# Performance work log

Hardware: AMD Instinct MI355X
Metric: run time of the kernel (lower is better)

Reference implementation:

```python
import jax, jax.numpy as jnp
import numpy as np

N = 100000
D_IN = 256
C = 4          # num_classes
D_C = 32       # output_dim // num_classes
E = 1600000    # nnz per class adjacency


def setup_inputs() -> dict:
    key = jax.random.key(0)
    k1, k2, k3, k4, k5 = jax.random.split(key, 5)
    x = jax.random.normal(k1, (N, D_IN), dtype=jnp.float32)
    # kernel (input_dim, output_dim) split along axis=1 into C chunks -> [D_IN, C, D_C]
    W = jax.random.normal(k2, (D_IN, C, D_C), dtype=jnp.float32) * (2.0 / D_IN) ** 0.5
    rows = jax.random.randint(k3, (C, E), 0, N, dtype=jnp.int64)
    cols = jax.random.randint(k4, (C, E), 0, N, dtype=jnp.int64)
    vals = jax.random.uniform(k5, (C, E), dtype=jnp.float32)
    return {"x": x, "W": W, "rows": rows, "cols": cols, "vals": vals}


def reference(x, W, rows, cols, vals):
    # dropout with rate 0.0 is identity.
    n = x.shape[0]
    # per-class dense transform: tmp[:, c, :] = x @ W[:, c, :]
    tmp = jnp.einsum('nd,dcf->ncf', x, W)  # [N, C, D_C]

    def prop(r, c, v, t):
        # t: [N, D_C] features for one class; SpMM A_c @ t via gather+segment_sum
        msg = t[c] * v[:, None]                              # [E, D_C]
        return jax.ops.segment_sum(msg, r, num_segments=n)   # [N, D_C]

    out = jax.vmap(prop, in_axes=(0, 0, 0, 1))(rows, cols, vals, tmp)  # [C, N, D_C]
    z = jnp.transpose(out, (1, 0, 2)).reshape(n, -1)  # concat along feature axis -> [N, C*D_C]
    return jax.nn.relu(z)
```

## Files before the change

kernel.cpp:

```cpp
#include <hip/hip_runtime.h>
#include <hip/hip_bf16.h>
#include <hip/hip_fp16.h>

#define D_IN 256
#define D_OUT 128
#define D_C 32
#define NUM_C 4
#define RB_LOG 10
#define RB 1024
#define MB_MAX 400

typedef _Float16 f16x8 __attribute__((ext_vector_type(8)));
typedef float    f32x4 __attribute__((ext_vector_type(4)));

__global__ void wcvt_kernel(const float* __restrict__ W, __half* __restrict__ Wt) {
    int t = blockIdx.x * 256 + threadIdx.x;
    if (t >= D_IN * D_OUT) return;
    int col = t >> 8;
    int k   = t & 255;
    Wt[col * D_IN + k] = __float2half(W[k * D_OUT + col]);
}

__global__ __launch_bounds__(256) void bucket_hist_kernel(const int* __restrict__ rows,
                                                          int* __restrict__ bcnt,
                                                          int CE, int E, int NB, int MB) {
    __shared__ int h[MB_MAX];
    const int t = threadIdx.x;
    for (int i = t; i < MB; i += 256) h[i] = 0;
    __syncthreads();
    const int CE4 = CE >> 2;
    const int4* rows4 = reinterpret_cast<const int4*>(rows);
    int base4 = blockIdx.x * 4096;
    #pragma unroll 4
    for (int i = 0; i < 16; ++i) {
        int i4 = base4 + t + i * 256;
        if (i4 < CE4) {
            int e0 = i4 << 2;
            int c = (e0 >= 3 * E) ? 3 : (e0 >= 2 * E) ? 2 : (e0 >= E) ? 1 : 0;
            int4 rv = rows4[i4];
            atomicAdd(&h[c * NB + (rv.x >> RB_LOG)], 1);
            atomicAdd(&h[c * NB + (rv.y >> RB_LOG)], 1);
            atomicAdd(&h[c * NB + (rv.z >> RB_LOG)], 1);
            atomicAdd(&h[c * NB + (rv.w >> RB_LOG)], 1);
        }
    }
    if (blockIdx.x == 0 && t < (CE & 3)) {
        int e = (CE4 << 2) + t;
        int c = (e >= 3 * E) ? 3 : (e >= 2 * E) ? 2 : (e >= E) ? 1 : 0;
        atomicAdd(&h[c * NB + (rows[e] >> RB_LOG)], 1);
    }
    __syncthreads();
    for (int i = t; i < MB; i += 256)
        if (h[i]) atomicAdd(&bcnt[i], h[i]);
}

__global__ __launch_bounds__(512) void bucket_scan_kernel(const int* __restrict__ bcnt,
                                                          int* __restrict__ bstartP,
                                                          int* __restrict__ bheadLine,
                                                          int* __restrict__ bstartD,
                                                          int* __restrict__ starts,
                                                          int MB, int M, int slackLines) {
    __shared__ int sd[512];
    int t = threadIdx.x;
    int v = (t < MB) ? bcnt[t] : 0;
    int capL = ((v + 7) >> 3) + slackLines;
    sd[t] = capL; __syncthreads();
    for (int off = 1; off < 512; off <<= 1) {
        int add = (t >= off) ? sd[t - off] : 0;
        __syncthreads();
        sd[t] += add;
        __syncthreads();
    }
    int exclL = sd[t] - capL;
    if (t < MB) { bstartP[t] = exclL * 8; bheadLine[t] = exclL; }
    __syncthreads();
    sd[t] = v; __syncthreads();
    for (int off = 1; off < 512; off <<= 1) {
        int add = (t >= off) ? sd[t - off] : 0;
        __syncthreads();
        sd[t] += add;
        __syncthreads();
    }
    int exclD = sd[t] - v;
    if (t < MB) bstartD[t] = exclD;
    if (t == 511) starts[M] = sd[511];
}

__global__ __launch_bounds__(512) void part_gemm_kernel(const int* __restrict__ rows,
                                                        const int* __restrict__ cols,
                                                        const float* __restrict__ vals,
                                                        int* __restrict__ bheadLine,
                                                        int2* __restrict__ arena,
                                                        int CE, int E, int NB, int MB,
                                                        int partBlocks,
                                                        const float* __restrict__ x,
                                                        const __half* __restrict__ Wt,
                                                        __half* __restrict__ tmp,
                                                        int Nrows) {
    __shared__ __align__(16) char smem[65536];
    const int t = threadIdx.x;

    if (blockIdx.x < partBlocks) {
        int* lcnt  = (int*)smem;
        int* lbase = lcnt + MB_MAX;
        for (int i = t; i < MB; i += 512) lcnt[i] = 0;
        __syncthreads();
        const int base = blockIdx.x * 8192;
        const int end  = min(base + 8192, CE);

        {
            int nvec4 = (end - base) >> 2;
            const int4* rows4 = reinterpret_cast<const int4*>(rows + base);
            #pragma unroll 4
            for (int i = 0; i < 4; ++i) {
                int i4 = t + i * 512;
                if (i4 < nvec4) {
                    int e0 = base + (i4 << 2);
                    int c = (e0 >= 3 * E) ? 3 : (e0 >= 2 * E) ? 2 : (e0 >= E) ? 1 : 0;
                    int4 rv = rows4[i4];
                    atomicAdd(&lcnt[c * NB + (rv.x >> RB_LOG)], 1);
                    atomicAdd(&lcnt[c * NB + (rv.y >> RB_LOG)], 1);
                    atomicAdd(&lcnt[c * NB + (rv.z >> RB_LOG)], 1);
                    atomicAdd(&lcnt[c * NB + (rv.w >> RB_LOG)], 1);
                }
            }
            int e = base + (nvec4 << 2) + t;
            if (e < end) {
                int c = (e >= 3 * E) ? 3 : (e >= 2 * E) ? 2 : (e >= E) ? 1 : 0;
                atomicAdd(&lcnt[c * NB + (rows[e] >> RB_LOG)], 1);
            }
        }
        __syncthreads();

        for (int b = t; b < MB; b += 512) {
            int n = lcnt[b];
            lbase[b] = n ? atomicAdd(&bheadLine[b], (n + 7) >> 3) * 8 : 0;
        }
        __syncthreads();
        for (int i = t; i < MB; i += 512) lcnt[i] = 0;
        __syncthreads();

        for (int i = 0; i < 16; ++i) {
            int e = base + t + i * 512;
            if (e < end) {
                int c = (e >= 3 * E) ? 3 : (e >= 2 * E) ? 2 : (e >= E) ? 1 : 0;
                int r = rows[e];
                int b = c * NB + (r >> RB_LOG);
                int rank = atomicAdd(&lcnt[b], 1);
                arena[lbase[b] + rank] = make_int2(cols[e] | ((r & (RB - 1)) << 17),
                                                   __float_as_int(vals[e]));
            }
        }
        __syncthreads();

        for (int b = t; b < MB; b += 512) {
            int n = lcnt[b];
            if (n) {
                int endp = ((n + 7) >> 3) * 8;
                for (int s2 = n; s2 < endp; ++s2)
                    arena[lbase[b] + s2] = make_int2(-1, 0);
            }
        }
    } else {
        f16x8* As = (f16x8*)smem;
        const int brow = (blockIdx.x - partBlocks) * 128;
        const int w   = t >> 6;
        const int cls = w & 3;
        const int rh  = w >> 2;
        const int l   = t & 63;
        const int l15 = l & 15;
        const int hi  = l >> 4;

        f16x8 bf[8][2];
        #pragma unroll
        for (int ks = 0; ks < 8; ++ks)
            #pragma unroll
            for (int cti = 0; cti < 2; ++cti)
                bf[ks][cti] = *reinterpret_cast<const f16x8*>(
                    Wt + (size_t)((cls * 2 + cti) * 16 + l15) * D_IN + ks * 32 + hi * 8);

        #pragma unroll
        for (int i = 0; i < 8; ++i) {
            int ci  = i * 512 + t;
            int row = ci >> 5;
            int kc  = ci & 31;
            int grow = brow + row;
            float4 a0 = make_float4(0.f, 0.f, 0.f, 0.f);
            float4 a1 = make_float4(0.f, 0.f, 0.f, 0.f);
            if (grow < Nrows) {
                const float* src = x + (size_t)grow * D_IN + kc * 8;
                a0 = *reinterpret_cast<const float4*>(src);
                a1 = *reinterpret_cast<const float4*>(src + 4);
            }
            f16x8 hh;
            hh[0] = (_Float16)a0.x; hh[1] = (_Float16)a0.y;
            hh[2] = (_Float16)a0.z; hh[3] = (_Float16)a0.w;
            hh[4] = (_Float16)a1.x; hh[5] = (_Float16)a1.y;
            hh[6] = (_Float16)a1.z; hh[7] = (_Float16)a1.w;
            As[kc * 128 + (row ^ kc)] = hh;
        }
        __syncthreads();

        f32x4 acc[4][2] = {};
        #pragma unroll
        for (int rt = 0; rt < 4; ++rt) {
            const int arow = rh * 64 + rt * 16 + l15;
            #pragma unroll
            for (int ks = 0; ks < 8; ++ks) {
                const int kcA = ks * 4 + hi;
                f16x8 afrag = As[kcA * 128 + (arow ^ kcA)];
                acc[rt][0] = __builtin_amdgcn_mfma_f32_16x16x32_f16(afrag, bf[ks][0], acc[rt][0], 0, 0, 0);
                acc[rt][1] = __builtin_amdgcn_mfma_f32_16x16x32_f16(afrag, bf[ks][1], acc[rt][1], 0, 0, 0);
            }
        }

        #pragma unroll
        for (int rt = 0; rt < 4; ++rt)
            #pragma unroll
            for (int cti = 0; cti < 2; ++cti) {
                const int cio = cti * 16 + l15;
                #pragma unroll
                for (int r = 0; r < 4; ++r) {
                    int grow = brow + rh * 64 + rt * 16 + hi * 4 + r;
                    if (grow < Nrows)
                        tmp[((size_t)cls * Nrows + grow) * 32 + cio] = __float2half((float)acc[rt][cti][r]);
                }
            }
    }
}

__global__ __launch_bounds__(1024) void rowsort_kernel(const int* __restrict__ bstartP,
                                                       const int* __restrict__ bheadLine,
                                                       const int* __restrict__ bstartD,
                                                       const int2* __restrict__ src,
                                                       unsigned* __restrict__ dst,
                                                       int* __restrict__ starts,
                                                       int N, int NB) {
    __shared__ int lcnt[RB];
    __shared__ int sd[RB];
    int b = blockIdx.x;
    int c = b / NB, rb = b - c * NB;
    int t = threadIdx.x;
    int s = bstartP[b];
    int nspan = bheadLine[b] * 8 - s;
    int dbase = bstartD[b];

    lcnt[t] = 0;
    __syncthreads();
    for (int i = t; i < nspan; i += 1024) {
        unsigned u = (unsigned)src[s + i].x;
        if ((u & 0x1FFFFu) != 0x1FFFFu)
            atomicAdd(&lcnt[(u >> 17) & (RB - 1)], 1);
    }
    __syncthreads();
    int v = lcnt[t];
    sd[t] = v; __syncthreads();
    for (int off = 1; off < 1024; off <<= 1) {
        int add = (t >= off) ? sd[t - off] : 0;
        __syncthreads();
        sd[t] += add;
        __syncthreads();
    }
    int excl = sd[t] - v;
    int grow = (rb << RB_LOG) + t;
    if (grow < N) starts[c * N + grow] = dbase + excl;
    __syncthreads();
    lcnt[t] = excl;
    __syncthreads();
    for (int i = t; i < nspan; i += 1024) {
        int2 rec = src[s + i];
        unsigned u = (unsigned)rec.x;
        if ((u & 0x1FFFFu) != 0x1FFFFu) {
            int rl  = (u >> 17) & (RB - 1);
            int pos = atomicAdd(&lcnt[rl], 1);
            __half h = __float2half(__int_as_float(rec.y));
            unsigned hb = (unsigned)*reinterpret_cast<unsigned short*>(&h);
            dst[dbase + pos] = (hb << 17) | (u & 0x1FFFFu);
        }
    }
}

__global__ __launch_bounds__(256) void pull2_kernel(const int* __restrict__ starts,
                                                    const unsigned* __restrict__ arena,
                                                    const uint2* __restrict__ tmp4,
                                                    float* __restrict__ out,
                                                    int N, int M) {
    int p = blockIdx.x * 32 + (threadIdx.x >> 3);
    if (p >= M) return;
    const int lf = threadIdx.x & 7;
    int c   = p / N;
    int row = p - c * N;
    int s = starts[p];
    int n = starts[p + 1] - s;
    const uint2* tc = tmp4 + (size_t)c * N * 8 + lf;

    float4 acc = make_float4(0.f, 0.f, 0.f, 0.f);
    int base = 0;
    for (; base + 16 <= n; base += 16) {
        unsigned r[16];
        #pragma unroll
        for (int j = 0; j < 16; ++j) r[j] = arena[s + base + j];
        #pragma unroll
        for (int j = 0; j < 16; ++j) {
            unsigned short hb = (unsigned short)(r[j] >> 17);
            float v = __half2float(*reinterpret_cast<__half*>(&hb));
            uint2 tw = tc[(size_t)(r[j] & 0x1FFFFu) * 8];
            float2 t0 = __half22float2(*reinterpret_cast<__half2*>(&tw.x));
            float2 t1 = __half22float2(*reinterpret_cast<__half2*>(&tw.y));
            acc.x = fmaf(v, t0.x, acc.x);
            acc.y = fmaf(v, t0.y, acc.y);
            acc.z = fmaf(v, t1.x, acc.z);
            acc.w = fmaf(v, t1.y, acc.w);
        }
    }
    if (base + 8 <= n) {
        unsigned r[8];
        #pragma unroll
        for (int j = 0; j < 8; ++j) r[j] = arena[s + base + j];
        #pragma unroll
        for (int j = 0; j < 8; ++j) {
            unsigned short hb = (unsigned short)(r[j] >> 17);
            float v = __half2float(*reinterpret_cast<__half*>(&hb));
            uint2 tw = tc[(size_t)(r[j] & 0x1FFFFu) * 8];
            float2 t0 = __half22float2(*reinterpret_cast<__half2*>(&tw.x));
            float2 t1 = __half22float2(*reinterpret_cast<__half2*>(&tw.y));
            acc.x = fmaf(v, t0.x, acc.x);
            acc.y = fmaf(v, t0.y, acc.y);
            acc.z = fmaf(v, t1.x, acc.z);
            acc.w = fmaf(v, t1.y, acc.w);
        }
        base += 8;
    }
    for (; base < n; ++base) {
        unsigned u = arena[s + base];
        unsigned short hb = (unsigned short)(u >> 17);
        float v = __half2float(*reinterpret_cast<__half*>(&hb));
        uint2 tw = tc[(size_t)(u & 0x1FFFFu) * 8];
        float2 t0 = __half22float2(*reinterpret_cast<__half2*>(&tw.x));
        float2 t1 = __half22float2(*reinterpret_cast<__half2*>(&tw.y));
        acc.x = fmaf(v, t0.x, acc.x);
        acc.y = fmaf(v, t0.y, acc.y);
        acc.z = fmaf(v, t1.x, acc.z);
        acc.w = fmaf(v, t1.y, acc.w);
    }
    *reinterpret_cast<float4*>(&out[(size_t)row * D_OUT + c * D_C + 4 * lf]) =
        make_float4(fmaxf(acc.x, 0.f), fmaxf(acc.y, 0.f),
                    fmaxf(acc.z, 0.f), fmaxf(acc.w, 0.f));
}

__global__ __launch_bounds__(256) void scatter_kernel(const int* __restrict__ rows,
                                                      const int* __restrict__ cols,
                                                      const float* __restrict__ vals,
                                                      const __half* __restrict__ tmp,
                                                      float* __restrict__ out,
                                                      long long totalEdges, int E, int N) {
    long long gid = (long long)blockIdx.x * 8 + (threadIdx.x >> 5);
    if (gid >= totalEdges) return;
    const int lane = threadIdx.x & 31;
    const long long e1 = E, e2 = 2LL * E, e3 = 3LL * E;
    int c = (gid >= e3) ? 3 : (gid >= e2) ? 2 : (gid >= e1) ? 1 : 0;
    const float tv = __half2float(tmp[((size_t)c * N + cols[gid]) * 32 + lane]);
    atomicAdd(&out[(size_t)rows[gid] * D_OUT + c * D_C + lane], tv * vals[gid]);
}

__global__ void relu_kernel(float* __restrict__ out, int n4) {
    int i = blockIdx.x * blockDim.x + threadIdx.x;
    if (i < n4) {
        float4 v = reinterpret_cast<float4*>(out)[i];
        v.x = fmaxf(v.x, 0.f); v.y = fmaxf(v.y, 0.f);
        v.z = fmaxf(v.z, 0.f); v.w = fmaxf(v.w, 0.f);
        reinterpret_cast<float4*>(out)[i] = v;
    }
}

extern "C" void kernel_launch(void* const* d_in, const int* in_sizes, int n_in,
                              void* d_out, int out_size, void* d_ws, size_t ws_size,
                              hipStream_t stream) {
    const float* x    = (const float*)d_in[0];
    const float* W    = (const float*)d_in[1];
    const int*   rows = (const int*)d_in[2];
    const int*   cols = (const int*)d_in[3];
    const float* vals = (const float*)d_in[4];
    float* out = (float*)d_out;

    const int N  = in_sizes[0] / D_IN;
    const int CE = in_sizes[2];
    const int E  = CE / NUM_C;
    const int NB = (N + RB - 1) >> RB_LOG;
    const int MB = NUM_C * NB;
    const int M  = NUM_C * N;

    const int partBlocks = (CE + 8191) / 8192;
    const int gemmBlocks = (N + 127) / 128;
    const int slackLines = (7 * partBlocks + 7) / 8 + 1;
    const long long capRecs = (long long)((CE + 7) & ~7) + (long long)MB * slackLines * 8 + (long long)MB * 8;

    size_t off = 0;
    __half* tmp  = (__half*)((char*)d_ws + off); off += (size_t)N * D_OUT * 2;
    off = (off + 15) & ~(size_t)15;
    __half* Wt   = (__half*)((char*)d_ws + off); off += (size_t)D_IN * D_OUT * 2;
    int* bcnt    = (int*)((char*)d_ws + off);   off += (size_t)MB * 4;
    int* bstartP = (int*)((char*)d_ws + off);   off += (size_t)MB * 4;
    int* bheadL  = (int*)((char*)d_ws + off);   off += (size_t)MB * 4;
    int* bstartD = (int*)((char*)d_ws + off);   off += (size_t)MB * 4;
    int* starts  = (int*)((char*)d_ws + off);   off += (size_t)(M + 1) * 4;
    off = (off + 63) & ~(size_t)63;
    int2* arena  = (int2*)((char*)d_ws + off);  off += (size_t)capRecs * 8;
    unsigned* sorted = (unsigned*)((char*)d_ws + off); off += (size_t)CE * 4;
    const bool ok = (off <= ws_size) && (MB <= MB_MAX) && (MB <= 512);

    wcvt_kernel<<<(D_IN * D_OUT + 255) / 256, 256, 0, stream>>>(W, Wt);

    if (ok) {
        hipMemsetAsync(bcnt, 0, (size_t)MB * 4, stream);
        const int histBlocks = ((CE >> 2) + 4095) / 4096;
        bucket_hist_kernel<<<histBlocks, 256, 0, stream>>>(rows, bcnt, CE, E, NB, MB);
        bucket_scan_kernel<<<1, 512, 0, stream>>>(bcnt, bstartP, bheadL, bstartD, starts, MB, M, slackLines);
        part_gemm_kernel<<<partBlocks + gemmBlocks, 512, 0, stream>>>(
            rows, cols, vals, bheadL, arena, CE, E, NB, MB, partBlocks, x, Wt, tmp, N);
        rowsort_kernel<<<MB, 1024, 0, stream>>>(bstartP, bheadL, bstartD, arena, sorted, starts, N, NB);
        const int pullBlocks = (M + 31) / 32;
        pull2_kernel<<<pullBlocks, 256, 0, stream>>>(starts, sorted,
                                                     reinterpret_cast<const uint2*>(tmp), out, N, M);
    } else {
        part_gemm_kernel<<<gemmBlocks, 512, 0, stream>>>(
            rows, cols, vals, bheadL, arena, CE, E, NB, MB, 0, x, Wt, tmp, N);
        hipMemsetAsync(d_out, 0, (size_t)out_size * sizeof(float), stream);
        const int scatterBlocks = (CE + 7) / 8;
        scatter_kernel<<<scatterBlocks, 256, 0, stream>>>(rows, cols, vals, tmp, out, (long long)CE, E, N);
        const int n4 = out_size / 4;
        relu_kernel<<<(n4 + 255) / 256, 256, 0, stream>>>(out, n4);
    }
}
```

Baseline: 274.8 us.

## Interleave partition and GEMM blocks and halve GEMM row tile

The fused partition/GEMM launch now interleaves block roles: every third block does edge partitioning and the other two do GEMM work. Before, all partition blocks came first and all GEMM blocks after. The GEMM tile shrinks from 128 to 64 rows, and shared memory drops from 64KB to 32KB, so more blocks can be resident per CU. The aim is to overlap the atomic- and memory-bound partitioning with the MFMA-bound transform, instead of running them as two phases. Correctness relies on the grid being sized so that twice the partition block count covers all GEMM tiles, which holds for these shapes but is not checked in general.

```diff
diff --git a/kernel.cpp b/kernel.cpp
--- a/kernel.cpp
+++ b/kernel.cpp
@@ -92,20 +92,34 @@
                                                         int* __restrict__ bheadLine,
                                                         int2* __restrict__ arena,
                                                         int CE, int E, int NB, int MB,
-                                                        int partBlocks,
+                                                        int partBlocks, int gemmBlocks,
                                                         const float* __restrict__ x,
                                                         const __half* __restrict__ Wt,
                                                         __half* __restrict__ tmp,
                                                         int Nrows) {
-    __shared__ __align__(16) char smem[65536];
+    __shared__ __align__(16) char smem[32768];
     const int t = threadIdx.x;
-
-    if (blockIdx.x < partBlocks) {
+    const int bid = blockIdx.x;
+
+    bool isPart; int pidx, gidx;
+    if (partBlocks > 0) {
+        isPart = (bid % 3) == 0;
+        pidx = bid / 3;
+        gidx = bid - pidx - 1;
+        if (isPart && pidx >= partBlocks) return;
+        if (!isPart && gidx >= gemmBlocks) return;
+    } else {
+        isPart = false;
+        gidx = bid;
+        if (gidx >= gemmBlocks) return;
+    }
+
+    if (isPart) {
         int* lcnt  = (int*)smem;
         int* lbase = lcnt + MB_MAX;
         for (int i = t; i < MB; i += 512) lcnt[i] = 0;
         __syncthreads();
-        const int base = blockIdx.x * 8192;
+        const int base = pidx * 8192;
         const int end  = min(base + 8192, CE);
 
         {
@@ -124,7 +138,7 @@
                     atomicAdd(&lcnt[c * NB + (rv.w >> RB_LOG)], 1);
                 }
             }
-            int e = base + (nvec4 << 2) + t;
+            int e = base + (((end - base) >> 2) << 2) + t;
             if (e < end) {
                 int c = (e >= 3 * E) ? 3 : (e >= 2 * E) ? 2 : (e >= E) ? 1 : 0;
                 atomicAdd(&lcnt[c * NB + (rows[e] >> RB_LOG)], 1);
@@ -163,7 +177,7 @@
         }
     } else {
         f16x8* As = (f16x8*)smem;
-        const int brow = (blockIdx.x - partBlocks) * 128;
+        const int brow = gidx * 64;
         const int w   = t >> 6;
         const int cls = w & 3;
         const int rh  = w >> 2;
@@ -180,7 +194,7 @@
                     Wt + (size_t)((cls * 2 + cti) * 16 + l15) * D_IN + ks * 32 + hi * 8);
 
         #pragma unroll
-        for (int i = 0; i < 8; ++i) {
+        for (int i = 0; i < 4; ++i) {
             int ci  = i * 512 + t;
             int row = ci >> 5;
             int kc  = ci & 31;
@@ -197,31 +211,31 @@
             hh[2] = (_Float16)a0.z; hh[3] = (_Float16)a0.w;
             hh[4] = (_Float16)a1.x; hh[5] = (_Float16)a1.y;
             hh[6] = (_Float16)a1.z; hh[7] = (_Float16)a1.w;
-            As[kc * 128 + (row ^ kc)] = hh;
-        }
-        __syncthreads();
-
-        f32x4 acc[4][2] = {};
-        #pragma unroll
-        for (int rt = 0; rt < 4; ++rt) {
-            const int arow = rh * 64 + rt * 16 + l15;
+            As[kc * 64 + (row ^ kc)] = hh;
+        }
+        __syncthreads();
+
+        f32x4 acc[2][2] = {};
+        #pragma unroll
+        for (int rt = 0; rt < 2; ++rt) {
+            const int arow = rh * 32 + rt * 16 + l15;
             #pragma unroll
             for (int ks = 0; ks < 8; ++ks) {
                 const int kcA = ks * 4 + hi;
-                f16x8 afrag = As[kcA * 128 + (arow ^ kcA)];
+                f16x8 afrag = As[kcA * 64 + (arow ^ kcA)];
                 acc[rt][0] = __builtin_amdgcn_mfma_f32_16x16x32_f16(afrag, bf[ks][0], acc[rt][0], 0, 0, 0);
                 acc[rt][1] = __builtin_amdgcn_mfma_f32_16x16x32_f16(afrag, bf[ks][1], acc[rt][1], 0, 0, 0);
             }
         }
 
         #pragma unroll
-        for (int rt = 0; rt < 4; ++rt)
+        for (int rt = 0; rt < 2; ++rt)
             #pragma unroll
             for (int cti = 0; cti < 2; ++cti) {
                 const int cio = cti * 16 + l15;
                 #pragma unroll
                 for (int r = 0; r < 4; ++r) {
-                    int grow = brow + rh * 64 + rt * 16 + hi * 4 + r;
+                    int grow = brow + rh * 32 + rt * 16 + hi * 4 + r;
                     if (grow < Nrows)
                         tmp[((size_t)cls * Nrows + grow) * 32 + cio] = __float2half((float)acc[rt][cti][r]);
                 }
@@ -391,7 +405,7 @@
     const int M  = NUM_C * N;
 
     const int partBlocks = (CE + 8191) / 8192;
-    const int gemmBlocks = (N + 127) / 128;
+    const int gemmBlocks = (N + 63) / 64;
     const int slackLines = (7 * partBlocks + 7) / 8 + 1;
     const long long capRecs = (long long)((CE + 7) & ~7) + (long long)MB * slackLines * 8 + (long long)MB * 8;
 
@@ -416,15 +430,16 @@
         const int histBlocks = ((CE >> 2) + 4095) / 4096;
         bucket_hist_kernel<<<histBlocks, 256, 0, stream>>>(rows, bcnt, CE, E, NB, MB);
         bucket_scan_kernel<<<1, 512, 0, stream>>>(bcnt, bstartP, bheadL, bstartD, starts, MB, M, slackLines);
-        part_gemm_kernel<<<partBlocks + gemmBlocks, 512, 0, stream>>>(
-            rows, cols, vals, bheadL, arena, CE, E, NB, MB, partBlocks, x, Wt, tmp, N);
+        const int totalBlocks = 3 * partBlocks;
+        part_gemm_kernel<<<totalBlocks, 512, 0, stream>>>(
+            rows, cols, vals, bheadL, arena, CE, E, NB, MB, partBlocks, gemmBlocks, x, Wt, tmp, N);
         rowsort_kernel<<<MB, 1024, 0, stream>>>(bstartP, bheadL, bstartD, arena, sorted, starts, N, NB);
         const int pullBlocks = (M + 31) / 32;
         pull2_kernel<<<pullBlocks, 256, 0, stream>>>(starts, sorted,
                                                      reinterpret_cast<const uint2*>(tmp), out, N, M);
     } else {
         part_gemm_kernel<<<gemmBlocks, 512, 0, stream>>>(
-            rows, cols, vals, bheadL, arena, CE, E, NB, MB, 0, x, Wt, tmp, N);
+            rows, cols, vals, bheadL, arena, CE, E, NB, MB, 0, gemmBlocks, x, Wt, tmp, N);
         hipMemsetAsync(d_out, 0, (size_t)out_size * sizeof(float), stream);
         const int scatterBlocks = (CE + 7) / 8;
         scatter_kernel<<<scatterBlocks, 256, 0, stream>>>(rows, cols, vals, tmp, out, (long long)CE, E, N);
```

Result: slower. 287.3 us (+4.5%).

## Split partition arena into packed records and row-local array, stash rows in registers

Applied to the files above, without the earlier changes.

The partition stage now writes a 4-byte packed record (fp16 value and column) plus a separate 2-byte local-row array, replacing the 8-byte int2 arena, and moves fp16 conversion earlier. Allocation granularity changes from 8-record lines to 16-record units. The row-sort kernel reads only the 2-byte row array for its histogram, keeps those row ids in a register stash for the scatter pass, and copies the precomputed records directly. The aim is to cut arena write and read traffic. The cost is extra register pressure from the stash and somewhat more padding slack.

```diff
diff --git a/kernel.cpp b/kernel.cpp
--- a/kernel.cpp
+++ b/kernel.cpp
@@ -9,6 +9,7 @@
 #define RB_LOG 10
 #define RB 1024
 #define MB_MAX 400
+#define RSTASH 24
 
 typedef _Float16 f16x8 __attribute__((ext_vector_type(8)));
 typedef float    f32x4 __attribute__((ext_vector_type(4)));
@@ -55,24 +56,24 @@
 }
 
 __global__ __launch_bounds__(512) void bucket_scan_kernel(const int* __restrict__ bcnt,
-                                                          int* __restrict__ bstartP,
-                                                          int* __restrict__ bheadLine,
+                                                          int* __restrict__ bstartU,
+                                                          int* __restrict__ bheadU,
                                                           int* __restrict__ bstartD,
                                                           int* __restrict__ starts,
-                                                          int MB, int M, int slackLines) {
+                                                          int MB, int M, int slackUnits) {
     __shared__ int sd[512];
     int t = threadIdx.x;
     int v = (t < MB) ? bcnt[t] : 0;
-    int capL = ((v + 7) >> 3) + slackLines;
-    sd[t] = capL; __syncthreads();
+    int capU = ((v + 15) >> 4) + slackUnits;
+    sd[t] = capU; __syncthreads();
     for (int off = 1; off < 512; off <<= 1) {
         int add = (t >= off) ? sd[t - off] : 0;
         __syncthreads();
         sd[t] += add;
         __syncthreads();
     }
-    int exclL = sd[t] - capL;
-    if (t < MB) { bstartP[t] = exclL * 8; bheadLine[t] = exclL; }
+    int exclU = sd[t] - capU;
+    if (t < MB) { bstartU[t] = exclU; bheadU[t] = exclU; }
     __syncthreads();
     sd[t] = v; __syncthreads();
     for (int off = 1; off < 512; off <<= 1) {
@@ -89,8 +90,9 @@
 __global__ __launch_bounds__(512) void part_gemm_kernel(const int* __restrict__ rows,
                                                         const int* __restrict__ cols,
                                                         const float* __restrict__ vals,
-                                                        int* __restrict__ bheadLine,
-                                                        int2* __restrict__ arena,
+                                                        int* __restrict__ bheadU,
+                                                        unsigned* __restrict__ rec,
+                                                        unsigned short* __restrict__ rl,
                                                         int CE, int E, int NB, int MB,
                                                         int partBlocks,
                                                         const float* __restrict__ x,
@@ -124,7 +126,7 @@
                     atomicAdd(&lcnt[c * NB + (rv.w >> RB_LOG)], 1);
                 }
             }
-            int e = base + (nvec4 << 2) + t;
+            int e = base + (((end - base) >> 2) << 2) + t;
             if (e < end) {
                 int c = (e >= 3 * E) ? 3 : (e >= 2 * E) ? 2 : (e >= E) ? 1 : 0;
                 atomicAdd(&lcnt[c * NB + (rows[e] >> RB_LOG)], 1);
@@ -134,7 +136,7 @@
 
         for (int b = t; b < MB; b += 512) {
             int n = lcnt[b];
-            lbase[b] = n ? atomicAdd(&bheadLine[b], (n + 7) >> 3) * 8 : 0;
+            lbase[b] = n ? atomicAdd(&bheadU[b], (n + 15) >> 4) * 16 : 0;
         }
         __syncthreads();
         for (int i = t; i < MB; i += 512) lcnt[i] = 0;
@@ -147,8 +149,11 @@
                 int r = rows[e];
                 int b = c * NB + (r >> RB_LOG);
                 int rank = atomicAdd(&lcnt[b], 1);
-                arena[lbase[b] + rank] = make_int2(cols[e] | ((r & (RB - 1)) << 17),
-                                                   __float_as_int(vals[e]));
+                int pos = lbase[b] + rank;
+                __half h = __float2half(vals[e]);
+                unsigned hb = (unsigned)*reinterpret_cast<unsigned short*>(&h);
+                rec[pos] = (hb << 17) | (unsigned)cols[e];
+                rl[pos]  = (unsigned short)(r & (RB - 1));
             }
         }
         __syncthreads();
@@ -156,9 +161,9 @@
         for (int b = t; b < MB; b += 512) {
             int n = lcnt[b];
             if (n) {
-                int endp = ((n + 7) >> 3) * 8;
+                int endp = ((n + 15) >> 4) << 4;
                 for (int s2 = n; s2 < endp; ++s2)
-                    arena[lbase[b] + s2] = make_int2(-1, 0);
+                    rl[lbase[b] + s2] = 0xFFFFu;
             }
         }
     } else {
@@ -229,10 +234,11 @@
     }
 }
 
-__global__ __launch_bounds__(1024) void rowsort_kernel(const int* __restrict__ bstartP,
-                                                       const int* __restrict__ bheadLine,
+__global__ __launch_bounds__(1024) void rowsort_kernel(const int* __restrict__ bstartU,
+                                                       const int* __restrict__ bheadU,
                                                        const int* __restrict__ bstartD,
-                                                       const int2* __restrict__ src,
+                                                       const unsigned short* __restrict__ rl,
+                                                       const unsigned* __restrict__ rec,
                                                        unsigned* __restrict__ dst,
                                                        int* __restrict__ starts,
                                                        int N, int NB) {
@@ -241,16 +247,25 @@
     int b = blockIdx.x;
     int c = b / NB, rb = b - c * NB;
     int t = threadIdx.x;
-    int s = bstartP[b];
-    int nspan = bheadLine[b] * 8 - s;
+    int s = bstartU[b] * 16;
+    int span = bheadU[b] * 16 - s;
     int dbase = bstartD[b];
 
+    unsigned short st[RSTASH];
     lcnt[t] = 0;
     __syncthreads();
-    for (int i = t; i < nspan; i += 1024) {
-        unsigned u = (unsigned)src[s + i].x;
-        if ((u & 0x1FFFFu) != 0x1FFFFu)
-            atomicAdd(&lcnt[(u >> 17) & (RB - 1)], 1);
+    #pragma unroll
+    for (int k = 0; k < RSTASH; ++k) {
+        int i = t + k * 1024;
+        if (i < span) {
+            unsigned short r = rl[s + i];
+            st[k] = r;
+            if (r < RB) atomicAdd(&lcnt[r], 1);
+        }
+    }
+    for (int i = t + RSTASH * 1024; i < span; i += 1024) {
+        unsigned short r = rl[s + i];
+        if (r < RB) atomicAdd(&lcnt[r], 1);
     }
     __syncthreads();
     int v = lcnt[t];
@@ -267,15 +282,22 @@
     __syncthreads();
     lcnt[t] = excl;
     __syncthreads();
-    for (int i = t; i < nspan; i += 1024) {
-        int2 rec = src[s + i];
-        unsigned u = (unsigned)rec.x;
-        if ((u & 0x1FFFFu) != 0x1FFFFu) {
-            int rl  = (u >> 17) & (RB - 1);
-            int pos = atomicAdd(&lcnt[rl], 1);
-            __half h = __float2half(__int_as_float(rec.y));
-            unsigned hb = (unsigned)*reinterpret_cast<unsigned short*>(&h);
-            dst[dbase + pos] = (hb << 17) | (u & 0x1FFFFu);
+    #pragma unroll
+    for (int k = 0; k < RSTASH; ++k) {
+        int i = t + k * 1024;
+        if (i < span) {
+            unsigned short r = st[k];
+            if (r < RB) {
+                int pos = atomicAdd(&lcnt[r], 1);
+                dst[dbase + pos] = rec[s + i];
+            }
+        }
+    }
+    for (int i = t + RSTASH * 1024; i < span; i += 1024) {
+        unsigned short r = rl[s + i];
+        if (r < RB) {
+            int pos = atomicAdd(&lcnt[r], 1);
+            dst[dbase + pos] = rec[s + i];
         }
     }
 }
@@ -392,21 +414,25 @@
 
     const int partBlocks = (CE + 8191) / 8192;
     const int gemmBlocks = (N + 127) / 128;
-    const int slackLines = (7 * partBlocks + 7) / 8 + 1;
-    const long long capRecs = (long long)((CE + 7) & ~7) + (long long)MB * slackLines * 8 + (long long)MB * 8;
+    const int slackUnits = (15 * partBlocks + 15) / 16 + 1;
+    const long long capRecs = (long long)((CE + 15) & ~15)
+                            + (long long)MB * slackUnits * 16 + (long long)MB * 16;
 
     size_t off = 0;
     __half* tmp  = (__half*)((char*)d_ws + off); off += (size_t)N * D_OUT * 2;
     off = (off + 15) & ~(size_t)15;
     __half* Wt   = (__half*)((char*)d_ws + off); off += (size_t)D_IN * D_OUT * 2;
     int* bcnt    = (int*)((char*)d_ws + off);   off += (size_t)MB * 4;
-    int* bstartP = (int*)((char*)d_ws + off);   off += (size_t)MB * 4;
-    int* bheadL  = (int*)((char*)d_ws + off);   off += (size_t)MB * 4;
+    int* bstartU = (int*)((char*)d_ws + off);   off += (size_t)MB * 4;
+    int* bheadU  = (int*)((char*)d_ws + off);   off += (size_t)MB * 4;
     int* bstartD = (int*)((char*)d_ws + off);   off += (size_t)MB * 4;
     int* starts  = (int*)((char*)d_ws + off);   off += (size_t)(M + 1) * 4;
     off = (off + 63) & ~(size_t)63;
-    int2* arena  = (int2*)((char*)d_ws + off);  off += (size_t)capRecs * 8;
-    unsigned* sorted = (unsigned*)((char*)d_ws + off); off += (size_t)CE * 4;
+    unsigned* rec = (unsigned*)((char*)d_ws + off);        off += (size_t)capRecs * 4;
+    off = (off + 63) & ~(size_t)63;
+    unsigned short* rlA = (unsigned short*)((char*)d_ws + off); off += (size_t)capRecs * 2;
+    off = (off + 63) & ~(size_t)63;
+    unsigned* sorted = (unsigned*)((char*)d_ws + off);     off += (size_t)CE * 4;
     const bool ok = (off <= ws_size) && (MB <= MB_MAX) && (MB <= 512);
 
     wcvt_kernel<<<(D_IN * D_OUT + 255) / 256, 256, 0, stream>>>(W, Wt);
@@ -415,16 +441,16 @@
         hipMemsetAsync(bcnt, 0, (size_t)MB * 4, stream);
         const int histBlocks = ((CE >> 2) + 4095) / 4096;
         bucket_hist_kernel<<<histBlocks, 256, 0, stream>>>(rows, bcnt, CE, E, NB, MB);
-        bucket_scan_kernel<<<1, 512, 0, stream>>>(bcnt, bstartP, bheadL, bstartD, starts, MB, M, slackLines);
+        bucket_scan_kernel<<<1, 512, 0, stream>>>(bcnt, bstartU, bheadU, bstartD, starts, MB, M, slackUnits);
         part_gemm_kernel<<<partBlocks + gemmBlocks, 512, 0, stream>>>(
-            rows, cols, vals, bheadL, arena, CE, E, NB, MB, partBlocks, x, Wt, tmp, N);
-        rowsort_kernel<<<MB, 1024, 0, stream>>>(bstartP, bheadL, bstartD, arena, sorted, starts, N, NB);
+            rows, cols, vals, bheadU, rec, rlA, CE, E, NB, MB, partBlocks, x, Wt, tmp, N);
+        rowsort_kernel<<<MB, 1024, 0, stream>>>(bstartU, bheadU, bstartD, rlA, rec, sorted, starts, N, NB);
         const int pullBlocks = (M + 31) / 32;
         pull2_kernel<<<pullBlocks, 256, 0, stream>>>(starts, sorted,
                                                      reinterpret_cast<const uint2*>(tmp), out, N, M);
     } else {
         part_gemm_kernel<<<gemmBlocks, 512, 0, stream>>>(
-            rows, cols, vals, bheadL, arena, CE, E, NB, MB, 0, x, Wt, tmp, N);
+            rows, cols, vals, bheadU, rec, rlA, CE, E, NB, MB, 0, x, Wt, tmp, N);
         hipMemsetAsync(d_out, 0, (size_t)out_size * sizeof(float), stream);
         const int scatterBlocks = (CE + 7) / 8;
         scatter_kernel<<<scatterBlocks, 256, 0, stream>>>(rows, cols, vals, tmp, out, (long long)CE, E, N);
```

New measurement: 310.9 us. 13.2% more time.

## Co-schedule part of GEMM with histogram pass and stash records in rowsort

Applied to the files above, without the earlier changes.

Moves the first 256 GEMM tiles into the histogram kernel, which now runs 512-thread blocks, so dense transform work overlaps the bucket counting pass. The partition kernel runs only the remaining GEMM tiles. Rowsort now keeps up to 20 records per thread in registers from the counting pass and reuses them in the scatter pass, so the arena is not read twice. The trade-off is higher register pressure in rowsort and a less even load balance between the hist and GEMM blocks.

```diff
diff --git a/kernel.cpp b/kernel.cpp
--- a/kernel.cpp
+++ b/kernel.cpp
@@ -9,6 +9,7 @@
 #define RB_LOG 10
 #define RB 1024
 #define MB_MAX 400
+#define RSTASH 20
 
 typedef _Float16 f16x8 __attribute__((ext_vector_type(8)));
 typedef float    f32x4 __attribute__((ext_vector_type(4)));
@@ -21,37 +22,120 @@
     Wt[col * D_IN + k] = __float2half(W[k * D_OUT + col]);
 }
 
-__global__ __launch_bounds__(256) void bucket_hist_kernel(const int* __restrict__ rows,
-                                                          int* __restrict__ bcnt,
-                                                          int CE, int E, int NB, int MB) {
-    __shared__ int h[MB_MAX];
+__device__ __forceinline__ void gemm_tile(const float* __restrict__ x,
+                                          const __half* __restrict__ Wt,
+                                          __half* __restrict__ tmp,
+                                          int Nrows, int gidx, char* smem, int t) {
+    f16x8* As = (f16x8*)smem;
+    const int brow = gidx * 128;
+    const int w   = t >> 6;
+    const int cls = w & 3;
+    const int rh  = w >> 2;
+    const int l   = t & 63;
+    const int l15 = l & 15;
+    const int hi  = l >> 4;
+
+    f16x8 bf[8][2];
+    #pragma unroll
+    for (int ks = 0; ks < 8; ++ks)
+        #pragma unroll
+        for (int cti = 0; cti < 2; ++cti)
+            bf[ks][cti] = *reinterpret_cast<const f16x8*>(
+                Wt + (size_t)((cls * 2 + cti) * 16 + l15) * D_IN + ks * 32 + hi * 8);
+
+    #pragma unroll
+    for (int i = 0; i < 8; ++i) {
+        int ci  = i * 512 + t;
+        int row = ci >> 5;
+        int kc  = ci & 31;
+        int grow = brow + row;
+        float4 a0 = make_float4(0.f, 0.f, 0.f, 0.f);
+        float4 a1 = make_float4(0.f, 0.f, 0.f, 0.f);
+        if (grow < Nrows) {
+            const float* src = x + (size_t)grow * D_IN + kc * 8;
+            a0 = *reinterpret_cast<const float4*>(src);
+            a1 = *reinterpret_cast<const float4*>(src + 4);
+        }
+        f16x8 hh;
+        hh[0] = (_Float16)a0.x; hh[1] = (_Float16)a0.y;
+        hh[2] = (_Float16)a0.z; hh[3] = (_Float16)a0.w;
+        hh[4] = (_Float16)a1.x; hh[5] = (_Float16)a1.y;
+        hh[6] = (_Float16)a1.z; hh[7] = (_Float16)a1.w;
+        As[kc * 128 + (row ^ kc)] = hh;
+    }
+    __syncthreads();
+
+    f32x4 acc[4][2] = {};
+    #pragma unroll
+    for (int rt = 0; rt < 4; ++rt) {
+        const int arow = rh * 64 + rt * 16 + l15;
+        #pragma unroll
+        for (int ks = 0; ks < 8; ++ks) {
+            const int kcA = ks * 4 + hi;
+            f16x8 afrag = As[kcA * 128 + (arow ^ kcA)];
+            acc[rt][0] = __builtin_amdgcn_mfma_f32_16x16x32_f16(afrag, bf[ks][0], acc[rt][0], 0, 0, 0);
+            acc[rt][1] = __builtin_amdgcn_mfma_f32_16x16x32_f16(afrag, bf[ks][1], acc[rt][1], 0, 0, 0);
+        }
+    }
+
+    #pragma unroll
+    for (int rt = 0; rt < 4; ++rt)
+        #pragma unroll
+        for (int cti = 0; cti < 2; ++cti) {
+            const int cio = cti * 16 + l15;
+            #pragma unroll
+            for (int r = 0; r < 4; ++r) {
+                int grow = brow + rh * 64 + rt * 16 + hi * 4 + r;
+                if (grow < Nrows)
+                    tmp[((size_t)cls * Nrows + grow) * 32 + cio] = __float2half((float)acc[rt][cti][r]);
+            }
+        }
+}
+
+__global__ __launch_bounds__(512) void hist_gemm_kernel(const int* __restrict__ rows,
+                                                        int* __restrict__ bcnt,
+                                                        int CE, int E, int NB, int MB,
+                                                        int histBlocks, int G1,
+                                                        const float* __restrict__ x,
+                                                        const __half* __restrict__ Wt,
+                                                        __half* __restrict__ tmp,
+                                                        int Nrows) {
+    __shared__ __align__(16) char smem[65536];
     const int t = threadIdx.x;
-    for (int i = t; i < MB; i += 256) h[i] = 0;
-    __syncthreads();
-    const int CE4 = CE >> 2;
-    const int4* rows4 = reinterpret_cast<const int4*>(rows);
-    int base4 = blockIdx.x * 4096;
-    #pragma unroll 4
-    for (int i = 0; i < 16; ++i) {
-        int i4 = base4 + t + i * 256;
-        if (i4 < CE4) {
-            int e0 = i4 << 2;
-            int c = (e0 >= 3 * E) ? 3 : (e0 >= 2 * E) ? 2 : (e0 >= E) ? 1 : 0;
-            int4 rv = rows4[i4];
-            atomicAdd(&h[c * NB + (rv.x >> RB_LOG)], 1);
-            atomicAdd(&h[c * NB + (rv.y >> RB_LOG)], 1);
-            atomicAdd(&h[c * NB + (rv.z >> RB_LOG)], 1);
-            atomicAdd(&h[c * NB + (rv.w >> RB_LOG)], 1);
-        }
-    }
-    if (blockIdx.x == 0 && t < (CE & 3)) {
-        int e = (CE4 << 2) + t;
-        int c = (e >= 3 * E) ? 3 : (e >= 2 * E) ? 2 : (e >= E) ? 1 : 0;
-        atomicAdd(&h[c * NB + (rows[e] >> RB_LOG)], 1);
-    }
-    __syncthreads();
-    for (int i = t; i < MB; i += 256)
-        if (h[i]) atomicAdd(&bcnt[i], h[i]);
+    const int bid = blockIdx.x;
+
+    if (bid < histBlocks) {
+        int* h = (int*)smem;
+        for (int i = t; i < MB; i += 512) h[i] = 0;
+        __syncthreads();
+        const int CE4 = CE >> 2;
+        const int4* rows4 = reinterpret_cast<const int4*>(rows);
+        int base4 = bid * 4096;
+        #pragma unroll 4
+        for (int i = 0; i < 8; ++i) {
+            int i4 = base4 + t + i * 512;
+            if (i4 < CE4) {
+                int e0 = i4 << 2;
+                int c = (e0 >= 3 * E) ? 3 : (e0 >= 2 * E) ? 2 : (e0 >= E) ? 1 : 0;
+                int4 rv = rows4[i4];
+                atomicAdd(&h[c * NB + (rv.x >> RB_LOG)], 1);
+                atomicAdd(&h[c * NB + (rv.y >> RB_LOG)], 1);
+                atomicAdd(&h[c * NB + (rv.z >> RB_LOG)], 1);
+                atomicAdd(&h[c * NB + (rv.w >> RB_LOG)], 1);
+            }
+        }
+        if (bid == 0 && t < (CE & 3)) {
+            int e = (CE4 << 2) + t;
+            int c = (e >= 3 * E) ? 3 : (e >= 2 * E) ? 2 : (e >= E) ? 1 : 0;
+            atomicAdd(&h[c * NB + (rows[e] >> RB_LOG)], 1);
+        }
+        __syncthreads();
+        for (int i = t; i < MB; i += 512)
+            if (h[i]) atomicAdd(&bcnt[i], h[i]);
+    } else {
+        int gidx = bid - histBlocks;
+        if (gidx < G1) gemm_tile(x, Wt, tmp, Nrows, gidx, smem, t);
+    }
 }
 
 __global__ __launch_bounds__(512) void bucket_scan_kernel(const int* __restrict__ bcnt,
@@ -92,7 +176,7 @@
                                                         int* __restrict__ bheadLine,
                                                         int2* __restrict__ arena,
                                                         int CE, int E, int NB, int MB,
-                                                        int partBlocks,
+                                                        int partBlocks, int G1, int gemmBlocks,
                                                         const float* __restrict__ x,
                                                         const __half* __restrict__ Wt,
                                                         __half* __restrict__ tmp,
@@ -124,7 +208,7 @@
                     atomicAdd(&lcnt[c * NB + (rv.w >> RB_LOG)], 1);
                 }
             }
-            int e = base + (nvec4 << 2) + t;
+            int e = base + (((end - base) >> 2) << 2) + t;
             if (e < end) {
                 int c = (e >= 3 * E) ? 3 : (e >= 2 * E) ? 2 : (e >= E) ? 1 : 0;
                 atomicAdd(&lcnt[c * NB + (rows[e] >> RB_LOG)], 1);
@@ -162,70 +246,8 @@
             }
         }
     } else {
-        f16x8* As = (f16x8*)smem;
-        const int brow = (blockIdx.x - partBlocks) * 128;
-        const int w   = t >> 6;
-        const int cls = w & 3;
-        const int rh  = w >> 2;
-        const int l   = t & 63;
-        const int l15 = l & 15;
-        const int hi  = l >> 4;
-
-        f16x8 bf[8][2];
-        #pragma unroll
-        for (int ks = 0; ks < 8; ++ks)
-            #pragma unroll
-            for (int cti = 0; cti < 2; ++cti)
-                bf[ks][cti] = *reinterpret_cast<const f16x8*>(
-                    Wt + (size_t)((cls * 2 + cti) * 16 + l15) * D_IN + ks * 32 + hi * 8);
-
-        #pragma unroll
-        for (int i = 0; i < 8; ++i) {
-            int ci  = i * 512 + t;
-            int row = ci >> 5;
-            int kc  = ci & 31;
-            int grow = brow + row;
-            float4 a0 = make_float4(0.f, 0.f, 0.f, 0.f);
-            float4 a1 = make_float4(0.f, 0.f, 0.f, 0.f);
-            if (grow < Nrows) {
-                const float* src = x + (size_t)grow * D_IN + kc * 8;
-                a0 = *reinterpret_cast<const float4*>(src);
-                a1 = *reinterpret_cast<const float4*>(src + 4);
-            }
-            f16x8 hh;
-            hh[0] = (_Float16)a0.x; hh[1] = (_Float16)a0.y;
-            hh[2] = (_Float16)a0.z; hh[3] = (_Float16)a0.w;
-            hh[4] = (_Float16)a1.x; hh[5] = (_Float16)a1.y;
-            hh[6] = (_Float16)a1.z; hh[7] = (_Float16)a1.w;
-            As[kc * 128 + (row ^ kc)] = hh;
-        }
-        __syncthreads();
-
-        f32x4 acc[4][2] = {};
-        #pragma unroll
-        for (int rt = 0; rt < 4; ++rt) {
-            const int arow = rh * 64 + rt * 16 + l15;
-            #pragma unroll
-            for (int ks = 0; ks < 8; ++ks) {
-                const int kcA = ks * 4 + hi;
-                f16x8 afrag = As[kcA * 128 + (arow ^ kcA)];
-                acc[rt][0] = __builtin_amdgcn_mfma_f32_16x16x32_f16(afrag, bf[ks][0], acc[rt][0], 0, 0, 0);
-                acc[rt][1] = __builtin_amdgcn_mfma_f32_16x16x32_f16(afrag, bf[ks][1], acc[rt][1], 0, 0, 0);
-            }
-        }
-
-        #pragma unroll
-        for (int rt = 0; rt < 4; ++rt)
-            #pragma unroll
-            for (int cti = 0; cti < 2; ++cti) {
-                const int cio = cti * 16 + l15;
-                #pragma unroll
-                for (int r = 0; r < 4; ++r) {
-                    int grow = brow + rh * 64 + rt * 16 + hi * 4 + r;
-                    if (grow < Nrows)
-                        tmp[((size_t)cls * Nrows + grow) * 32 + cio] = __float2half((float)acc[rt][cti][r]);
-                }
-            }
+        int gidx = G1 + (blockIdx.x - partBlocks);
+        if (gidx < gemmBlocks) gemm_tile(x, Wt, tmp, Nrows, gidx, smem, t);
     }
 }
 
@@ -245,9 +267,21 @@
     int nspan = bheadLine[b] * 8 - s;
     int dbase = bstartD[b];
 
+    int2 st[RSTASH];
     lcnt[t] = 0;
     __syncthreads();
-    for (int i = t; i < nspan; i += 1024) {
+    #pragma unroll
+    for (int k = 0; k < RSTASH; ++k) {
+        int i = t + k * 1024;
+        if (i < nspan) {
+            int2 rec = src[s + i];
+            st[k] = rec;
+            unsigned u = (unsigned)rec.x;
+            if ((u & 0x1FFFFu) != 0x1FFFFu)
+                atomicAdd(&lcnt[(u >> 17) & (RB - 1)], 1);
+        }
+    }
+    for (int i = t + RSTASH * 1024; i < nspan; i += 1024) {
         unsigned u = (unsigned)src[s + i].x;
         if ((u & 0x1FFFFu) != 0x1FFFFu)
             atomicAdd(&lcnt[(u >> 17) & (RB - 1)], 1);
@@ -267,7 +301,22 @@
     __syncthreads();
     lcnt[t] = excl;
     __syncthreads();
-    for (int i = t; i < nspan; i += 1024) {
+    #pragma unroll
+    for (int k = 0; k < RSTASH; ++k) {
+        int i = t + k * 1024;
+        if (i < nspan) {
+            int2 rec = st[k];
+            unsigned u = (unsigned)rec.x;
+            if ((u & 0x1FFFFu) != 0x1FFFFu) {
+                int rl  = (u >> 17) & (RB - 1);
+                int pos = atomicAdd(&lcnt[rl], 1);
+                __half h = __float2half(__int_as_float(rec.y));
+                unsigned hb = (unsigned)*reinterpret_cast<unsigned short*>(&h);
+                dst[dbase + pos] = (hb << 17) | (u & 0x1FFFFu);
+            }
+        }
+    }
+    for (int i = t + RSTASH * 1024; i < nspan; i += 1024) {
         int2 rec = src[s + i];
         unsigned u = (unsigned)rec.x;
         if ((u & 0x1FFFFu) != 0x1FFFFu) {
@@ -392,6 +441,7 @@
 
     const int partBlocks = (CE + 8191) / 8192;
     const int gemmBlocks = (N + 127) / 128;
+    const int G1 = min(256, gemmBlocks);
     const int slackLines = (7 * partBlocks + 7) / 8 + 1;
     const long long capRecs = (long long)((CE + 7) & ~7) + (long long)MB * slackLines * 8 + (long long)MB * 8;
 
@@ -411,20 +461,22 @@
 
     wcvt_kernel<<<(D_IN * D_OUT + 255) / 256, 256, 0, stream>>>(W, Wt);
 
+    const int histBlocks = ((CE >> 2) + 4095) / 4096;
+
     if (ok) {
         hipMemsetAsync(bcnt, 0, (size_t)MB * 4, stream);
-        const int histBlocks = ((CE >> 2) + 4095) / 4096;
-        bucket_hist_kernel<<<histBlocks, 256, 0, stream>>>(rows, bcnt, CE, E, NB, MB);
+        hist_gemm_kernel<<<histBlocks + G1, 512, 0, stream>>>(
+            rows, bcnt, CE, E, NB, MB, histBlocks, G1, x, Wt, tmp, N);
         bucket_scan_kernel<<<1, 512, 0, stream>>>(bcnt, bstartP, bheadL, bstartD, starts, MB, M, slackLines);
-        part_gemm_kernel<<<partBlocks + gemmBlocks, 512, 0, stream>>>(
-            rows, cols, vals, bheadL, arena, CE, E, NB, MB, partBlocks, x, Wt, tmp, N);
+        part_gemm_kernel<<<partBlocks + (gemmBlocks - G1), 512, 0, stream>>>(
+            rows, cols, vals, bheadL, arena, CE, E, NB, MB, partBlocks, G1, gemmBlocks, x, Wt, tmp, N);
         rowsort_kernel<<<MB, 1024, 0, stream>>>(bstartP, bheadL, bstartD, arena, sorted, starts, N, NB);
         const int pullBlocks = (M + 31) / 32;
         pull2_kernel<<<pullBlocks, 256, 0, stream>>>(starts, sorted,
                                                      reinterpret_cast<const uint2*>(tmp), out, N, M);
     } else {
         part_gemm_kernel<<<gemmBlocks, 512, 0, stream>>>(
-            rows, cols, vals, bheadL, arena, CE, E, NB, MB, 0, x, Wt, tmp, N);
+            rows, cols, vals, bheadL, arena, CE, E, NB, MB, 0, 0, gemmBlocks, x, Wt, tmp, N);
         hipMemsetAsync(d_out, 0, (size_t)out_size * sizeof(float), stream);
         const int scatterBlocks = (CE + 7) / 8;
         scatter_kernel<<<scatterBlocks, 256, 0, stream>>>(rows, cols, vals, tmp, out, (long long)CE, E, N);
```

Measured after the change: 267.2 us. 2.7% less time.
